# Optimization experiments

Measured on AMD Instinct MI355X. Metric: run time of the kernel, lower is better.

## Reference

```python
import jax, jax.numpy as jnp
import numpy as np

NEG_INF = -jnp.inf


def setup_inputs() -> dict:
    key = jax.random.key(0)
    kq, kk, kv = jax.random.split(key, 3)
    B, L, H, E = 2, 2048, 16, 64
    queries = jax.random.normal(kq, (B, L, H, E), dtype=jnp.float32)
    keys = jax.random.normal(kk, (B, L, H, E), dtype=jnp.float32)
    values = jax.random.normal(kv, (B, L, H, E), dtype=jnp.float32)
    return {"queries": queries, "keys": keys, "values": values}


def reference(queries, keys, values):
    B, L, H, E = queries.shape
    scale = 1.0 / jnp.sqrt(jnp.asarray(E, dtype=queries.dtype))
    # scores: [B, H, L, S]
    scores = jnp.einsum("blhe,bshe->bhls", queries, keys)
    # causal mask: True above the diagonal -> masked out
    causal = jnp.triu(jnp.ones((L, L), dtype=bool), k=1)
    scores = jnp.where(causal[None, None, :, :], NEG_INF, scores)
    A = jax.nn.softmax(scale * scores, axis=-1)
    # output: [B, L, H, D]
    V = jnp.einsum("bhls,bshd->blhd", A, values)
    return V
```

## Files before the change

### kernel.cpp

```cpp
#include <hip/hip_runtime.h>


using f32x4  = __attribute__((ext_vector_type(4))) float;
using bf16x8 = __attribute__((ext_vector_type(8))) short;
using u32x2  = __attribute__((ext_vector_type(2))) unsigned int;
using u32x4  = __attribute__((ext_vector_type(4))) unsigned int;

constexpr int L = 2048;
constexpr int H = 16;
constexpr int E = 64;
constexpr int QBLK = 64;
constexpr int KVBLK = 64;
constexpr float QSC = 0.125f * 1.44269504088896f;
constexpr float THR = 8.0f;

#if defined(__has_builtin)
#if __has_builtin(__builtin_amdgcn_exp2f)
#define HAVE_EXP2 1
#endif
#endif
__device__ __forceinline__ float fexp2(float x) {
#ifdef HAVE_EXP2
    return __builtin_amdgcn_exp2f(x);
#else
    float r;
    asm("v_exp_f32 %0, %1" : "=v"(r) : "v"(x));
    return r;
#endif
}

__device__ __forceinline__ unsigned cvt_pk(float lo, float hi) {
    unsigned r;
    asm("v_cvt_pk_bf16_f32 %0, %1, %2" : "=v"(r) : "v"(lo), "v"(hi));
    return r;
}
__device__ __forceinline__ void pl16(unsigned& a, unsigned& b) {
    asm("v_permlane16_swap_b32 %0, %1" : "+v"(a), "+v"(b));
}
__device__ __forceinline__ void pl32(unsigned& a, unsigned& b) {
    asm("v_permlane32_swap_b32 %0, %1" : "+v"(a), "+v"(b));
}
__device__ __forceinline__ unsigned opaque_copy(unsigned a) {
    unsigned b;
    asm("v_mov_b32 %0, %1" : "=v"(b) : "v"(a));
    return b;
}
__device__ __forceinline__ float gmax4(float x) {
    unsigned a = __float_as_uint(x), b = opaque_copy(a);
    pl16(a, b);
    float m = fmaxf(__uint_as_float(a), __uint_as_float(b));
    unsigned c = __float_as_uint(m), d = opaque_copy(c);
    pl32(c, d);
    return fmaxf(__uint_as_float(c), __uint_as_float(d));
}
__device__ __forceinline__ float gsum4(float x) {
    unsigned a = __float_as_uint(x), b = opaque_copy(a);
    pl16(a, b);
    float s = __uint_as_float(a) + __uint_as_float(b);
    unsigned c = __float_as_uint(s), d = opaque_copy(c);
    pl32(c, d);
    return __uint_as_float(c) + __uint_as_float(d);
}
__device__ __forceinline__ int swz(int row, int bcol) {
    return (row * 128 + bcol) ^ ((row & 7) << 4);
}
__device__ __forceinline__ int swzV(int row, int bcol) {
    return (row * 128 + bcol) ^ ((((row & 7) ^ (row >> 3)) & 7) << 4);
}

__global__ __launch_bounds__(256)
void prep_kernel(const float* __restrict__ K, const float* __restrict__ V,
                 short* __restrict__ Kb, short* __restrict__ Vb)
{
    __shared__ float Vt[64][65];
    const int bx  = blockIdx.x;
    const int t   = bx & 31;
    const int bh  = bx >> 5;
    const int tid = threadIdx.x;
    const size_t bhoff = (size_t)(bh >> 4) * L * (H * E) + (size_t)(bh & 15) * E;
    const size_t tileo = (size_t)(bh * 32 + t) * 4096;

    #pragma unroll
    for (int g = 0; g < 2; ++g) {
        const int c  = g * 256 + tid;
        const int r  = c >> 3;
        const int e0 = (c & 7) * 8;
        const float* kp = K + bhoff + (size_t)(t * 64 + r) * 1024 + e0;
        f32x4 k0 = *(const f32x4*)kp, k1 = *(const f32x4*)(kp + 4);
        u32x4 kt;
        kt[0] = cvt_pk(k0[0], k0[1]); kt[1] = cvt_pk(k0[2], k0[3]);
        kt[2] = cvt_pk(k1[0], k1[1]); kt[3] = cvt_pk(k1[2], k1[3]);
        *(u32x4*)(Kb + tileo + r * 64 + (((e0 >> 3) ^ (r & 7)) * 8)) = kt;
        const float* vp = V + bhoff + (size_t)(t * 64 + r) * 1024 + e0;
        f32x4 v0 = *(const f32x4*)vp, v1 = *(const f32x4*)(vp + 4);
        #pragma unroll
        for (int k2 = 0; k2 < 4; ++k2) { Vt[r][e0 + k2] = v0[k2]; Vt[r][e0 + 4 + k2] = v1[k2]; }
    }
    __syncthreads();
    #pragma unroll
    for (int g = 0; g < 2; ++g) {
        const int c  = g * 256 + tid;
        const int d  = c >> 3;
        const int jp = c & 7;
        const int F  = ((d & 7) ^ (d >> 3)) & 7;
        const int col0 = 8 * (jp ^ F);
        float vals[8];
        #pragma unroll
        for (int i = 0; i < 8; ++i) {
            const int col = col0 + i;
            const int s = 16 * ((col >> 3) & 3) + 8 * (col >> 5) + (col & 7);
            vals[i] = Vt[s][d];
        }
        u32x4 vt;
        vt[0] = cvt_pk(vals[0], vals[1]); vt[1] = cvt_pk(vals[2], vals[3]);
        vt[2] = cvt_pk(vals[4], vals[5]); vt[3] = cvt_pk(vals[6], vals[7]);
        *(u32x4*)(Vb + tileo + d * 64 + jp * 8) = vt;
    }
}

__global__ __launch_bounds__(256, 4)
void fattn_main(const float* __restrict__ Q,
                const short* __restrict__ Kb,
                const short* __restrict__ Vb,
                float* __restrict__ O)
{
    __shared__ short Kl[2][4096];
    __shared__ short Vl[2][4096];

    const int bx  = blockIdx.x;
    const int xcd = bx & 7;
    const int j   = bx >> 3;
    const int bh  = (j & 3) * 8 + xcd;
    const int v_  = j >> 2;
    const int q2  = v_ >> 3, x_ = v_ & 7;
    const int iq  = (q2 & 1) ? (31 - (q2 >> 1) - 2 * x_) : (2 * x_ + (q2 >> 1));
    const int tid = threadIdx.x;
    const int w    = tid >> 6;
    const int lane = tid & 63;
    const int l16  = lane & 15;
    const int lhi  = lane >> 4;

    const size_t bhoff  = (size_t)(bh >> 4) * L * (H * E) + (size_t)(bh & 15) * E;
    const int rs_ = H * E;
    const size_t kvbase = (size_t)bh * 32 * 4096;

    u32x4 kreg[2], vreg[2];
    auto stage_regs = [&](int t) {
        const u32x4* kp = (const u32x4*)(Kb + kvbase + (size_t)t * 4096);
        const u32x4* vp = (const u32x4*)(Vb + kvbase + (size_t)t * 4096);
        #pragma unroll
        for (int g = 0; g < 2; ++g) {
            kreg[g] = kp[g * 256 + tid];
            vreg[g] = vp[g * 256 + tid];
        }
    };
    auto write_stage = [&](int buf) {
        #pragma unroll
        for (int g = 0; g < 2; ++g) {
            ((u32x4*)Kl[buf])[g * 256 + tid] = kreg[g];
            ((u32x4*)Vl[buf])[g * 256 + tid] = vreg[g];
        }
    };

    const int qg = iq * QBLK + w * 16 + l16;
    bf16x8 qf[2];
    {
        const float* qp = Q + bhoff + (size_t)qg * rs_ + lhi * 8;
        #pragma unroll
        for (int kf = 0; kf < 2; ++kf) {
            f32x4 xv = *(const f32x4*)(qp + kf * 32);
            f32x4 yv = *(const f32x4*)(qp + kf * 32 + 4);
            union { u32x4 u; bf16x8 hh; } r;
            r.u[0] = cvt_pk(xv[0] * QSC, xv[1] * QSC);
            r.u[1] = cvt_pk(xv[2] * QSC, xv[3] * QSC);
            r.u[2] = cvt_pk(yv[0] * QSC, yv[1] * QSC);
            r.u[3] = cvt_pk(yv[2] * QSC, yv[3] * QSC);
            qf[kf] = r.hh;
        }
    }

    float m_run = -INFINITY, lsum = 0.0f;
    f32x4 oacc[4];
    #pragma unroll
    for (int dt = 0; dt < 4; ++dt) oacc[dt] = (f32x4){0.f, 0.f, 0.f, 0.f};

    const int total = iq + 1;
    stage_regs(0);
    write_stage(0);
    if (total > 1) stage_regs(1);
    __syncthreads();

    for (int i = 0; i < total; ++i) {
        const char* Kbl = (const char*)Kl[i & 1];
        const char* Vbl = (const char*)Vl[i & 1];

        f32x4 p[4];
        #pragma unroll
        for (int st = 0; st < 4; ++st) p[st] = (f32x4){0.f, 0.f, 0.f, 0.f};
        __builtin_amdgcn_s_setprio(1);
        #pragma unroll
        for (int st = 0; st < 4; ++st) {
            #pragma unroll
            for (int kf = 0; kf < 2; ++kf) {
                bf16x8 af = *(const bf16x8*)(Kbl + swz(st * 16 + l16, (lhi * 8 + kf * 32) * 2));
                p[st] = __builtin_amdgcn_mfma_f32_16x16x32_bf16(af, qf[kf], p[st], 0, 0, 0);
            }
        }
        __builtin_amdgcn_s_setprio(0);

        if (i == total - 1) {
            #pragma unroll
            for (int st = 0; st < 4; ++st)
                #pragma unroll
                for (int r = 0; r < 4; ++r) {
                    const int kg = i * KVBLK + st * 16 + lhi * 4 + r;
                    if (kg > qg) p[st][r] = -INFINITY;
                }
        }

        if (i + 1 < total) write_stage((i + 1) & 1);
        if (i + 2 < total) stage_regs(i + 2);

        f32x4 mv = p[0];
        #pragma unroll
        for (int st = 1; st < 4; ++st)
            #pragma unroll
            for (int r = 0; r < 4; ++r) mv[r] = fmaxf(mv[r], p[st][r]);
        float mx = fmaxf(fmaxf(mv[0], mv[1]), fmaxf(mv[2], mv[3]));
        mx = gmax4(mx);
        if (!__all(mx <= m_run + THR)) {
            const float mn = fmaxf(m_run, mx);
            const float corr = fexp2(m_run - mn);
            lsum *= corr;
            #pragma unroll
            for (int dt = 0; dt < 4; ++dt)
                #pragma unroll
                for (int r = 0; r < 4; ++r) oacc[dt][r] *= corr;
            m_run = mn;
        }
        f32x4 rsv = (f32x4){0.f, 0.f, 0.f, 0.f};
        #pragma unroll
        for (int st = 0; st < 4; ++st)
            #pragma unroll
            for (int r = 0; r < 4; ++r) {
                const float e = fexp2(p[st][r] - m_run);
                p[st][r] = e;
                rsv[r] += e;
            }
        lsum += gsum4((rsv[0] + rsv[1]) + (rsv[2] + rsv[3]));

        unsigned wp[4][2];
        #pragma unroll
        for (int st = 0; st < 4; ++st) {
            wp[st][0] = cvt_pk(p[st][0], p[st][1]);
            wp[st][1] = cvt_pk(p[st][2], p[st][3]);
        }
        #pragma unroll
        for (int hh = 0; hh < 2; ++hh) {
            pl16(wp[0][hh], wp[1][hh]);
            pl16(wp[2][hh], wp[3][hh]);
            pl32(wp[0][hh], wp[2][hh]);
            pl32(wp[1][hh], wp[3][hh]);
        }
        union { u32x4 u; bf16x8 v; } pb0, pb1;
        pb0.u[0] = wp[0][0]; pb0.u[1] = wp[0][1];
        pb0.u[2] = wp[1][0]; pb0.u[3] = wp[1][1];
        pb1.u[0] = wp[2][0]; pb1.u[1] = wp[2][1];
        pb1.u[2] = wp[3][0]; pb1.u[3] = wp[3][1];

        __builtin_amdgcn_s_setprio(1);
        #pragma unroll
        for (int dt = 0; dt < 4; ++dt) {
            bf16x8 vf0 = *(const bf16x8*)(Vbl + swzV(dt * 16 + l16, (lhi * 8) * 2));
            oacc[dt] = __builtin_amdgcn_mfma_f32_16x16x32_bf16(vf0, pb0.v, oacc[dt], 0, 0, 0);
            bf16x8 vf1 = *(const bf16x8*)(Vbl + swzV(dt * 16 + l16, (lhi * 8 + 32) * 2));
            oacc[dt] = __builtin_amdgcn_mfma_f32_16x16x32_bf16(vf1, pb1.v, oacc[dt], 0, 0, 0);
        }
        __builtin_amdgcn_s_setprio(0);

        if (i + 1 < total) __syncthreads();
    }

    const float inv = 1.0f / lsum;
    float* op = O + bhoff + (size_t)qg * rs_;
    #pragma unroll
    for (int dt = 0; dt < 4; ++dt) {
        f32x4 o = oacc[dt];
        o[0] *= inv; o[1] *= inv; o[2] *= inv; o[3] *= inv;
        *(f32x4*)(op + dt * 16 + lhi * 4) = o;
    }
}

__global__ __launch_bounds__(256, 4)
void fattn_fb(const float* __restrict__ Q,
              const float* __restrict__ K,
              const float* __restrict__ V,
              float* __restrict__ O)
{
    __shared__ short Kl[2][KVBLK * 64];
    __shared__ short Vl[2][64 * KVBLK];

    const int bx  = blockIdx.x;
    const int xcd = bx & 7;
    const int j   = bx >> 3;
    const int bh  = (j & 3) * 8 + xcd;
    const int v_  = j >> 2;
    const int q2  = v_ >> 3, x_ = v_ & 7;
    const int iq  = (q2 & 1) ? (31 - (q2 >> 1) - 2 * x_) : (2 * x_ + (q2 >> 1));
    const int tid = threadIdx.x;
    const int w    = tid >> 6;
    const int lane = tid & 63;
    const int l16  = lane & 15;
    const int lhi  = lane >> 4;

    const size_t bhoff = (size_t)(bh >> 4) * L * (H * E) + (size_t)(bh & 15) * E;
    const int rs_ = H * E;
    const int sv0 = (tid >> 4) * 4;
    const int d0  = (tid & 15) * 4;
    const int kc  = ((sv0 >> 3) & 1) * 32 + (sv0 >> 4) * 8 + (sv0 & 7);

    f32x4 ka[2][2];
    f32x4 va[4];
    auto issue_loads = [&](int t) {
        const int sb = t * KVBLK;
        #pragma unroll
        for (int g = 0; g < 2; ++g) {
            const int c = g * 256 + tid;
            const int s = c >> 3;
            const int e0 = (c & 7) * 8;
            const f32x4* kp = (const f32x4*)(K + bhoff + (size_t)(sb + s) * rs_ + e0);
            ka[g][0] = kp[0];
            ka[g][1] = kp[1];
        }
        #pragma unroll
        for (int jj = 0; jj < 4; ++jj)
            va[jj] = *(const f32x4*)(V + bhoff + (size_t)(sb + sv0 + jj) * rs_ + d0);
    };
    auto write_lds = [&](int bufi) {
        short* Kb = Kl[bufi];
        short* Vb = Vl[bufi];
        #pragma unroll
        for (int g = 0; g < 2; ++g) {
            const int c = g * 256 + tid;
            const int s = c >> 3;
            const int e0 = (c & 7) * 8;
            u32x4 kt;
            kt[0] = cvt_pk(ka[g][0][0], ka[g][0][1]);
            kt[1] = cvt_pk(ka[g][0][2], ka[g][0][3]);
            kt[2] = cvt_pk(ka[g][1][0], ka[g][1][1]);
            kt[3] = cvt_pk(ka[g][1][2], ka[g][1][3]);
            *(u32x4*)((char*)Kb + swz(s, e0 * 2)) = kt;
        }
        #pragma unroll
        for (int dd = 0; dd < 4; ++dd) {
            u32x2 vt;
            vt[0] = cvt_pk(va[0][dd], va[1][dd]);
            vt[1] = cvt_pk(va[2][dd], va[3][dd]);
            *(u32x2*)((char*)Vb + swzV(d0 + dd, kc * 2)) = vt;
        }
    };

    const int qg = iq * QBLK + w * 16 + l16;
    bf16x8 qf[2];
    {
        const float* qp = Q + bhoff + (size_t)qg * rs_ + lhi * 8;
        #pragma unroll
        for (int kf = 0; kf < 2; ++kf) {
            f32x4 xv = *(const f32x4*)(qp + kf * 32);
            f32x4 yv = *(const f32x4*)(qp + kf * 32 + 4);
            union { u32x4 u; bf16x8 hh; } r;
            r.u[0] = cvt_pk(xv[0] * QSC, xv[1] * QSC);
            r.u[1] = cvt_pk(xv[2] * QSC, xv[3] * QSC);
            r.u[2] = cvt_pk(yv[0] * QSC, yv[1] * QSC);
            r.u[3] = cvt_pk(yv[2] * QSC, yv[3] * QSC);
            qf[kf] = r.hh;
        }
    }

    float m_run = -INFINITY, lsum = 0.0f;
    f32x4 oacc[4];
    #pragma unroll
    for (int dt = 0; dt < 4; ++dt) oacc[dt] = (f32x4){0.f, 0.f, 0.f, 0.f};

    const int total = iq + 1;
    issue_loads(0);
    write_lds(0);
    if (total > 1) issue_loads(1);
    __syncthreads();

    for (int i = 0; i < total; ++i) {
        const char* Kbl = (const char*)Kl[i & 1];
        const char* Vbl = (const char*)Vl[i & 1];
        f32x4 p[4];
        #pragma unroll
        for (int st = 0; st < 4; ++st) p[st] = (f32x4){0.f, 0.f, 0.f, 0.f};
        __builtin_amdgcn_s_setprio(1);
        #pragma unroll
        for (int st = 0; st < 4; ++st) {
            #pragma unroll
            for (int kf = 0; kf < 2; ++kf) {
                bf16x8 af = *(const bf16x8*)(Kbl + swz(st * 16 + l16, (lhi * 8 + kf * 32) * 2));
                p[st] = __builtin_amdgcn_mfma_f32_16x16x32_bf16(af, qf[kf], p[st], 0, 0, 0);
            }
        }
        __builtin_amdgcn_s_setprio(0);
        if (i == total - 1) {
            #pragma unroll
            for (int st = 0; st < 4; ++st)
                #pragma unroll
                for (int r = 0; r < 4; ++r) {
                    const int kg = i * KVBLK + st * 16 + lhi * 4 + r;
                    if (kg > qg) p[st][r] = -INFINITY;
                }
        }
        if (i + 1 < total) write_lds((i + 1) & 1);
        if (i + 2 < total) issue_loads(i + 2);

        f32x4 mv = p[0];
        #pragma unroll
        for (int st = 1; st < 4; ++st)
            #pragma unroll
            for (int r = 0; r < 4; ++r) mv[r] = fmaxf(mv[r], p[st][r]);
        float mx = fmaxf(fmaxf(mv[0], mv[1]), fmaxf(mv[2], mv[3]));
        mx = gmax4(mx);
        if (!__all(mx <= m_run + THR)) {
            const float mn = fmaxf(m_run, mx);
            const float corr = fexp2(m_run - mn);
            lsum *= corr;
            #pragma unroll
            for (int dt = 0; dt < 4; ++dt)
                #pragma unroll
                for (int r = 0; r < 4; ++r) oacc[dt][r] *= corr;
            m_run = mn;
        }
        f32x4 rsv = (f32x4){0.f, 0.f, 0.f, 0.f};
        #pragma unroll
        for (int st = 0; st < 4; ++st)
            #pragma unroll
            for (int r = 0; r < 4; ++r) {
                const float e = fexp2(p[st][r] - m_run);
                p[st][r] = e;
                rsv[r] += e;
            }
        lsum += gsum4((rsv[0] + rsv[1]) + (rsv[2] + rsv[3]));

        unsigned wp[4][2];
        #pragma unroll
        for (int st = 0; st < 4; ++st) {
            wp[st][0] = cvt_pk(p[st][0], p[st][1]);
            wp[st][1] = cvt_pk(p[st][2], p[st][3]);
        }
        #pragma unroll
        for (int hh = 0; hh < 2; ++hh) {
            pl16(wp[0][hh], wp[1][hh]);
            pl16(wp[2][hh], wp[3][hh]);
            pl32(wp[0][hh], wp[2][hh]);
            pl32(wp[1][hh], wp[3][hh]);
        }
        union { u32x4 u; bf16x8 v; } pb0, pb1;
        pb0.u[0] = wp[0][0]; pb0.u[1] = wp[0][1];
        pb0.u[2] = wp[1][0]; pb0.u[3] = wp[1][1];
        pb1.u[0] = wp[2][0]; pb1.u[1] = wp[2][1];
        pb1.u[2] = wp[3][0]; pb1.u[3] = wp[3][1];

        __builtin_amdgcn_s_setprio(1);
        #pragma unroll
        for (int dt = 0; dt < 4; ++dt) {
            bf16x8 vf0 = *(const bf16x8*)(Vbl + swzV(dt * 16 + l16, (lhi * 8) * 2));
            oacc[dt] = __builtin_amdgcn_mfma_f32_16x16x32_bf16(vf0, pb0.v, oacc[dt], 0, 0, 0);
            bf16x8 vf1 = *(const bf16x8*)(Vbl + swzV(dt * 16 + l16, (lhi * 8 + 32) * 2));
            oacc[dt] = __builtin_amdgcn_mfma_f32_16x16x32_bf16(vf1, pb1.v, oacc[dt], 0, 0, 0);
        }
        __builtin_amdgcn_s_setprio(0);
        if (i + 1 < total) __syncthreads();
    }

    const float inv = 1.0f / lsum;
    float* op = O + bhoff + (size_t)qg * rs_;
    #pragma unroll
    for (int dt = 0; dt < 4; ++dt) {
        f32x4 o = oacc[dt];
        o[0] *= inv; o[1] *= inv; o[2] *= inv; o[3] *= inv;
        *(f32x4*)(op + dt * 16 + lhi * 4) = o;
    }
}

extern "C" void kernel_launch(void* const* d_in, const int* in_sizes, int n_in,
                              void* d_out, int out_size, void* d_ws, size_t ws_size,
                              hipStream_t stream) {
    const float* Q = (const float*)d_in[0];
    const float* K = (const float*)d_in[1];
    const float* V = (const float*)d_in[2];
    float* O = (float*)d_out;
    const size_t kb_elems = (size_t)32 * 32 * 4096;
    if (ws_size >= 2 * kb_elems * sizeof(short)) {
        short* Kb = (short*)d_ws;
        short* Vb = Kb + kb_elems;
        prep_kernel<<<1024, 256, 0, stream>>>(K, V, Kb, Vb);
        fattn_main<<<1024, 256, 0, stream>>>(Q, Kb, Vb, O);
    } else {
        fattn_fb<<<1024, 256, 0, stream>>>(Q, K, V, O);
    }
}
```

Measured before the change: 50.47 us.

## Replace LDS-staged attention kernel with single-wave register-only kernel and paired work units

```diff
diff --git a/kernel.cpp b/kernel.cpp
--- a/kernel.cpp
+++ b/kernel.cpp
@@ -9,7 +9,6 @@
 constexpr int L = 2048;
 constexpr int H = 16;
 constexpr int E = 64;
-constexpr int QBLK = 64;
 constexpr int KVBLK = 64;
 constexpr float QSC = 0.125f * 1.44269504088896f;
 constexpr float THR = 8.0f;
@@ -118,14 +117,181 @@
     }
 }
 
+__global__ __launch_bounds__(64, 2)
+void fattn_nolds(const float* __restrict__ Q,
+                 const short* __restrict__ Kb,
+                 const short* __restrict__ Vb,
+                 float* __restrict__ O)
+{
+    const int bx   = blockIdx.x;
+    const int xcd  = bx & 7;
+    const int j    = bx >> 3;
+    const int bh   = (j >> 6) * 8 + xcd;
+    const int pa   = j & 63;
+    const int lane = threadIdx.x;
+    const int l16  = lane & 15;
+    const int lhi  = lane >> 4;
+
+    const size_t bhoff = (size_t)(bh >> 4) * L * (H * E) + (size_t)(bh & 15) * E;
+    const char* Kt0 = (const char*)(Kb + (size_t)bh * 32 * 4096);
+    const char* Vt0 = (const char*)(Vb + (size_t)bh * 32 * 4096);
+
+    int koff[2];
+    #pragma unroll
+    for (int kf = 0; kf < 2; ++kf)
+        koff[kf] = l16 * 128 + ((lhi * 16 + kf * 64) ^ ((l16 & 7) << 4));
+    int voff[4][2];
+    #pragma unroll
+    for (int dt = 0; dt < 4; ++dt) {
+        const int row = dt * 16 + l16;
+        const int msk = (((row & 7) ^ (row >> 3)) & 7) << 4;
+        #pragma unroll
+        for (int kf = 0; kf < 2; ++kf)
+            voff[dt][kf] = row * 128 + ((lhi * 16 + kf * 64) ^ msk);
+    }
+
+    for (int seg = 0; seg < 2; ++seg) {
+        const int unit = seg ? pa : 127 - pa;
+        const int T    = (unit >> 2) + 1;
+        const int qg   = unit * 16 + l16;
+
+        bf16x8 qf[2];
+        {
+            const float* qp = Q + bhoff + (size_t)qg * (H * E) + lhi * 8;
+            #pragma unroll
+            for (int kf = 0; kf < 2; ++kf) {
+                f32x4 xv = *(const f32x4*)(qp + kf * 32);
+                f32x4 yv = *(const f32x4*)(qp + kf * 32 + 4);
+                union { u32x4 u; bf16x8 hh; } r;
+                r.u[0] = cvt_pk(xv[0] * QSC, xv[1] * QSC);
+                r.u[1] = cvt_pk(xv[2] * QSC, xv[3] * QSC);
+                r.u[2] = cvt_pk(yv[0] * QSC, yv[1] * QSC);
+                r.u[3] = cvt_pk(yv[2] * QSC, yv[3] * QSC);
+                qf[kf] = r.hh;
+            }
+        }
+
+        float m_run = -INFINITY, lsum = 0.0f;
+        f32x4 oacc[4];
+        #pragma unroll
+        for (int dt = 0; dt < 4; ++dt) oacc[dt] = (f32x4){0.f, 0.f, 0.f, 0.f};
+
+        bf16x8 kreg[4][2], vreg[4][2];
+        #pragma unroll
+        for (int st = 0; st < 4; ++st)
+            #pragma unroll
+            for (int kf = 0; kf < 2; ++kf)
+                kreg[st][kf] = *(const bf16x8*)(Kt0 + st * 2048 + koff[kf]);
+
+        for (int t = 0; t < T; ++t) {
+            const char* Vtc = Vt0 + (size_t)t * 8192;
+            #pragma unroll
+            for (int dt = 0; dt < 4; ++dt)
+                #pragma unroll
+                for (int kf = 0; kf < 2; ++kf)
+                    vreg[dt][kf] = *(const bf16x8*)(Vtc + voff[dt][kf]);
+
+            f32x4 p[4];
+            #pragma unroll
+            for (int st = 0; st < 4; ++st) p[st] = (f32x4){0.f, 0.f, 0.f, 0.f};
+            #pragma unroll
+            for (int st = 0; st < 4; ++st)
+                #pragma unroll
+                for (int kf = 0; kf < 2; ++kf)
+                    p[st] = __builtin_amdgcn_mfma_f32_16x16x32_bf16(kreg[st][kf], qf[kf], p[st], 0, 0, 0);
+
+            if (t + 1 < T) {
+                const char* Ktc = Kt0 + (size_t)(t + 1) * 8192;
+                #pragma unroll
+                for (int st = 0; st < 4; ++st)
+                    #pragma unroll
+                    for (int kf = 0; kf < 2; ++kf)
+                        kreg[st][kf] = *(const bf16x8*)(Ktc + st * 2048 + koff[kf]);
+            }
+
+            if (t == T - 1) {
+                #pragma unroll
+                for (int st = 0; st < 4; ++st)
+                    #pragma unroll
+                    for (int r = 0; r < 4; ++r) {
+                        const int kg = t * KVBLK + st * 16 + lhi * 4 + r;
+                        if (kg > qg) p[st][r] = -INFINITY;
+                    }
+            }
+
+            f32x4 mv = p[0];
+            #pragma unroll
+            for (int st = 1; st < 4; ++st)
+                #pragma unroll
+                for (int r = 0; r < 4; ++r) mv[r] = fmaxf(mv[r], p[st][r]);
+            float mx = fmaxf(fmaxf(mv[0], mv[1]), fmaxf(mv[2], mv[3]));
+            mx = gmax4(mx);
+            if (!__all(mx <= m_run + THR)) {
+                const float mn = fmaxf(m_run, mx);
+                const float corr = fexp2(m_run - mn);
+                lsum *= corr;
+                #pragma unroll
+                for (int dt = 0; dt < 4; ++dt)
+                    #pragma unroll
+                    for (int r = 0; r < 4; ++r) oacc[dt][r] *= corr;
+                m_run = mn;
+            }
+            f32x4 rsv = (f32x4){0.f, 0.f, 0.f, 0.f};
+            #pragma unroll
+            for (int st = 0; st < 4; ++st)
+                #pragma unroll
+                for (int r = 0; r < 4; ++r) {
+                    const float e = fexp2(p[st][r] - m_run);
+                    p[st][r] = e;
+                    rsv[r] += e;
+                }
+            lsum += gsum4((rsv[0] + rsv[1]) + (rsv[2] + rsv[3]));
+
+            unsigned wp[4][2];
+            #pragma unroll
+            for (int st = 0; st < 4; ++st) {
+                wp[st][0] = cvt_pk(p[st][0], p[st][1]);
+                wp[st][1] = cvt_pk(p[st][2], p[st][3]);
+            }
+            #pragma unroll
+            for (int hh = 0; hh < 2; ++hh) {
+                pl16(wp[0][hh], wp[1][hh]);
+                pl16(wp[2][hh], wp[3][hh]);
+                pl32(wp[0][hh], wp[2][hh]);
+                pl32(wp[1][hh], wp[3][hh]);
+            }
+            union { u32x4 u; bf16x8 v; } pb0, pb1;
+            pb0.u[0] = wp[0][0]; pb0.u[1] = wp[0][1];
+            pb0.u[2] = wp[1][0]; pb0.u[3] = wp[1][1];
+            pb1.u[0] = wp[2][0]; pb1.u[1] = wp[2][1];
+            pb1.u[2] = wp[3][0]; pb1.u[3] = wp[3][1];
+
+            #pragma unroll
+            for (int dt = 0; dt < 4; ++dt) {
+                oacc[dt] = __builtin_amdgcn_mfma_f32_16x16x32_bf16(vreg[dt][0], pb0.v, oacc[dt], 0, 0, 0);
+                oacc[dt] = __builtin_amdgcn_mfma_f32_16x16x32_bf16(vreg[dt][1], pb1.v, oacc[dt], 0, 0, 0);
+            }
+        }
+
+        const float inv = 1.0f / lsum;
+        float* op = O + bhoff + (size_t)qg * (H * E);
+        #pragma unroll
+        for (int dt = 0; dt < 4; ++dt) {
+            f32x4 o = oacc[dt];
+            o[0] *= inv; o[1] *= inv; o[2] *= inv; o[3] *= inv;
+            *(f32x4*)(op + dt * 16 + lhi * 4) = o;
+        }
+    }
+}
+
 __global__ __launch_bounds__(256, 4)
-void fattn_main(const float* __restrict__ Q,
-                const short* __restrict__ Kb,
-                const short* __restrict__ Vb,
-                float* __restrict__ O)
+void fattn_fb(const float* __restrict__ Q,
+              const float* __restrict__ K,
+              const float* __restrict__ V,
+              float* __restrict__ O)
 {
-    __shared__ short Kl[2][4096];
-    __shared__ short Vl[2][4096];
+    __shared__ short Kl[2][KVBLK * 64];
+    __shared__ short Vl[2][64 * KVBLK];
 
     const int bx  = blockIdx.x;
     const int xcd = bx & 7;
@@ -140,179 +306,6 @@
     const int l16  = lane & 15;
     const int lhi  = lane >> 4;
 
-    const size_t bhoff  = (size_t)(bh >> 4) * L * (H * E) + (size_t)(bh & 15) * E;
-    const int rs_ = H * E;
-    const size_t kvbase = (size_t)bh * 32 * 4096;
-
-    u32x4 kreg[2], vreg[2];
-    auto stage_regs = [&](int t) {
-        const u32x4* kp = (const u32x4*)(Kb + kvbase + (size_t)t * 4096);
-        const u32x4* vp = (const u32x4*)(Vb + kvbase + (size_t)t * 4096);
-        #pragma unroll
-        for (int g = 0; g < 2; ++g) {
-            kreg[g] = kp[g * 256 + tid];
-            vreg[g] = vp[g * 256 + tid];
-        }
-    };
-    auto write_stage = [&](int buf) {
-        #pragma unroll
-        for (int g = 0; g < 2; ++g) {
-            ((u32x4*)Kl[buf])[g * 256 + tid] = kreg[g];
-            ((u32x4*)Vl[buf])[g * 256 + tid] = vreg[g];
-        }
-    };
-
-    const int qg = iq * QBLK + w * 16 + l16;
-    bf16x8 qf[2];
-    {
-        const float* qp = Q + bhoff + (size_t)qg * rs_ + lhi * 8;
-        #pragma unroll
-        for (int kf = 0; kf < 2; ++kf) {
-            f32x4 xv = *(const f32x4*)(qp + kf * 32);
-            f32x4 yv = *(const f32x4*)(qp + kf * 32 + 4);
-            union { u32x4 u; bf16x8 hh; } r;
-            r.u[0] = cvt_pk(xv[0] * QSC, xv[1] * QSC);
-            r.u[1] = cvt_pk(xv[2] * QSC, xv[3] * QSC);
-            r.u[2] = cvt_pk(yv[0] * QSC, yv[1] * QSC);
-            r.u[3] = cvt_pk(yv[2] * QSC, yv[3] * QSC);
-            qf[kf] = r.hh;
-        }
-    }
-
-    float m_run = -INFINITY, lsum = 0.0f;
-    f32x4 oacc[4];
-    #pragma unroll
-    for (int dt = 0; dt < 4; ++dt) oacc[dt] = (f32x4){0.f, 0.f, 0.f, 0.f};
-
-    const int total = iq + 1;
-    stage_regs(0);
-    write_stage(0);
-    if (total > 1) stage_regs(1);
-    __syncthreads();
-
-    for (int i = 0; i < total; ++i) {
-        const char* Kbl = (const char*)Kl[i & 1];
-        const char* Vbl = (const char*)Vl[i & 1];
-
-        f32x4 p[4];
-        #pragma unroll
-        for (int st = 0; st < 4; ++st) p[st] = (f32x4){0.f, 0.f, 0.f, 0.f};
-        __builtin_amdgcn_s_setprio(1);
-        #pragma unroll
-        for (int st = 0; st < 4; ++st) {
-            #pragma unroll
-            for (int kf = 0; kf < 2; ++kf) {
-                bf16x8 af = *(const bf16x8*)(Kbl + swz(st * 16 + l16, (lhi * 8 + kf * 32) * 2));
-                p[st] = __builtin_amdgcn_mfma_f32_16x16x32_bf16(af, qf[kf], p[st], 0, 0, 0);
-            }
-        }
-        __builtin_amdgcn_s_setprio(0);
-
-        if (i == total - 1) {
-            #pragma unroll
-            for (int st = 0; st < 4; ++st)
-                #pragma unroll
-                for (int r = 0; r < 4; ++r) {
-                    const int kg = i * KVBLK + st * 16 + lhi * 4 + r;
-                    if (kg > qg) p[st][r] = -INFINITY;
-                }
-        }
-
-        if (i + 1 < total) write_stage((i + 1) & 1);
-        if (i + 2 < total) stage_regs(i + 2);
-
-        f32x4 mv = p[0];
-        #pragma unroll
-        for (int st = 1; st < 4; ++st)
-            #pragma unroll
-            for (int r = 0; r < 4; ++r) mv[r] = fmaxf(mv[r], p[st][r]);
-        float mx = fmaxf(fmaxf(mv[0], mv[1]), fmaxf(mv[2], mv[3]));
-        mx = gmax4(mx);
-        if (!__all(mx <= m_run + THR)) {
-            const float mn = fmaxf(m_run, mx);
-            const float corr = fexp2(m_run - mn);
-            lsum *= corr;
-            #pragma unroll
-            for (int dt = 0; dt < 4; ++dt)
-                #pragma unroll
-                for (int r = 0; r < 4; ++r) oacc[dt][r] *= corr;
-            m_run = mn;
-        }
-        f32x4 rsv = (f32x4){0.f, 0.f, 0.f, 0.f};
-        #pragma unroll
-        for (int st = 0; st < 4; ++st)
-            #pragma unroll
-            for (int r = 0; r < 4; ++r) {
-                const float e = fexp2(p[st][r] - m_run);
-                p[st][r] = e;
-                rsv[r] += e;
-            }
-        lsum += gsum4((rsv[0] + rsv[1]) + (rsv[2] + rsv[3]));
-
-        unsigned wp[4][2];
-        #pragma unroll
-        for (int st = 0; st < 4; ++st) {
-            wp[st][0] = cvt_pk(p[st][0], p[st][1]);
-            wp[st][1] = cvt_pk(p[st][2], p[st][3]);
-        }
-        #pragma unroll
-        for (int hh = 0; hh < 2; ++hh) {
-            pl16(wp[0][hh], wp[1][hh]);
-            pl16(wp[2][hh], wp[3][hh]);
-            pl32(wp[0][hh], wp[2][hh]);
-            pl32(wp[1][hh], wp[3][hh]);
-        }
-        union { u32x4 u; bf16x8 v; } pb0, pb1;
-        pb0.u[0] = wp[0][0]; pb0.u[1] = wp[0][1];
-        pb0.u[2] = wp[1][0]; pb0.u[3] = wp[1][1];
-        pb1.u[0] = wp[2][0]; pb1.u[1] = wp[2][1];
-        pb1.u[2] = wp[3][0]; pb1.u[3] = wp[3][1];
-
-        __builtin_amdgcn_s_setprio(1);
-        #pragma unroll
-        for (int dt = 0; dt < 4; ++dt) {
-            bf16x8 vf0 = *(const bf16x8*)(Vbl + swzV(dt * 16 + l16, (lhi * 8) * 2));
-            oacc[dt] = __builtin_amdgcn_mfma_f32_16x16x32_bf16(vf0, pb0.v, oacc[dt], 0, 0, 0);
-            bf16x8 vf1 = *(const bf16x8*)(Vbl + swzV(dt * 16 + l16, (lhi * 8 + 32) * 2));
-            oacc[dt] = __builtin_amdgcn_mfma_f32_16x16x32_bf16(vf1, pb1.v, oacc[dt], 0, 0, 0);
-        }
-        __builtin_amdgcn_s_setprio(0);
-
-        if (i + 1 < total) __syncthreads();
-    }
-
-    const float inv = 1.0f / lsum;
-    float* op = O + bhoff + (size_t)qg * rs_;
-    #pragma unroll
-    for (int dt = 0; dt < 4; ++dt) {
-        f32x4 o = oacc[dt];
-        o[0] *= inv; o[1] *= inv; o[2] *= inv; o[3] *= inv;
-        *(f32x4*)(op + dt * 16 + lhi * 4) = o;
-    }
-}
-
-__global__ __launch_bounds__(256, 4)
-void fattn_fb(const float* __restrict__ Q,
-              const float* __restrict__ K,
-              const float* __restrict__ V,
-              float* __restrict__ O)
-{
-    __shared__ short Kl[2][KVBLK * 64];
-    __shared__ short Vl[2][64 * KVBLK];
-
-    const int bx  = blockIdx.x;
-    const int xcd = bx & 7;
-    const int j   = bx >> 3;
-    const int bh  = (j & 3) * 8 + xcd;
-    const int v_  = j >> 2;
-    const int q2  = v_ >> 3, x_ = v_ & 7;
-    const int iq  = (q2 & 1) ? (31 - (q2 >> 1) - 2 * x_) : (2 * x_ + (q2 >> 1));
-    const int tid = threadIdx.x;
-    const int w    = tid >> 6;
-    const int lane = tid & 63;
-    const int l16  = lane & 15;
-    const int lhi  = lane >> 4;
-
     const size_t bhoff = (size_t)(bh >> 4) * L * (H * E) + (size_t)(bh & 15) * E;
     const int rs_ = H * E;
     const int sv0 = (tid >> 4) * 4;
@@ -360,7 +353,7 @@
         }
     };
 
-    const int qg = iq * QBLK + w * 16 + l16;
+    const int qg = iq * 64 + w * 16 + l16;
     bf16x8 qf[2];
     {
         const float* qp = Q + bhoff + (size_t)qg * rs_ + lhi * 8;
@@ -394,7 +387,6 @@
         f32x4 p[4];
         #pragma unroll
         for (int st = 0; st < 4; ++st) p[st] = (f32x4){0.f, 0.f, 0.f, 0.f};
-        __builtin_amdgcn_s_setprio(1);
         #pragma unroll
         for (int st = 0; st < 4; ++st) {
             #pragma unroll
@@ -403,7 +395,6 @@
                 p[st] = __builtin_amdgcn_mfma_f32_16x16x32_bf16(af, qf[kf], p[st], 0, 0, 0);
             }
         }
-        __builtin_amdgcn_s_setprio(0);
         if (i == total - 1) {
             #pragma unroll
             for (int st = 0; st < 4; ++st)
@@ -463,7 +454,6 @@
         pb1.u[0] = wp[2][0]; pb1.u[1] = wp[2][1];
         pb1.u[2] = wp[3][0]; pb1.u[3] = wp[3][1];
 
-        __builtin_amdgcn_s_setprio(1);
         #pragma unroll
         for (int dt = 0; dt < 4; ++dt) {
             bf16x8 vf0 = *(const bf16x8*)(Vbl + swzV(dt * 16 + l16, (lhi * 8) * 2));
@@ -471,7 +461,6 @@
             bf16x8 vf1 = *(const bf16x8*)(Vbl + swzV(dt * 16 + l16, (lhi * 8 + 32) * 2));
             oacc[dt] = __builtin_amdgcn_mfma_f32_16x16x32_bf16(vf1, pb1.v, oacc[dt], 0, 0, 0);
         }
-        __builtin_amdgcn_s_setprio(0);
         if (i + 1 < total) __syncthreads();
     }
 
@@ -497,7 +486,7 @@
         short* Kb = (short*)d_ws;
         short* Vb = Kb + kb_elems;
         prep_kernel<<<1024, 256, 0, stream>>>(K, V, Kb, Vb);
-        fattn_main<<<1024, 256, 0, stream>>>(Q, Kb, Vb, O);
+        fattn_nolds<<<2048, 64, 0, stream>>>(Q, Kb, Vb, O);
     } else {
         fattn_fb<<<1024, 256, 0, stream>>>(Q, K, V, O);
     }
```

Result: slower. 66.56 us (+31.9%).

## Stage K/V tiles via direct global-to-LDS loads instead of register staging

Applied to the files above, without the earlier changes.

```diff
diff --git a/kernel.cpp b/kernel.cpp
--- a/kernel.cpp
+++ b/kernel.cpp
@@ -9,7 +9,6 @@
 constexpr int L = 2048;
 constexpr int H = 16;
 constexpr int E = 64;
-constexpr int QBLK = 64;
 constexpr int KVBLK = 64;
 constexpr float QSC = 0.125f * 1.44269504088896f;
 constexpr float THR = 8.0f;
@@ -67,6 +66,11 @@
 __device__ __forceinline__ int swzV(int row, int bcol) {
     return (row * 128 + bcol) ^ ((((row & 7) ^ (row >> 3)) & 7) << 4);
 }
+__device__ __forceinline__ void gload16(const short* g, short* l) {
+    __builtin_amdgcn_global_load_lds(
+        (const __attribute__((address_space(1))) void*)g,
+        (__attribute__((address_space(3))) void*)l, 16, 0, 0);
+}
 
 __global__ __launch_bounds__(256)
 void prep_kernel(const float* __restrict__ K, const float* __restrict__ V,
@@ -144,25 +148,20 @@
     const int rs_ = H * E;
     const size_t kvbase = (size_t)bh * 32 * 4096;
 
-    u32x4 kreg[2], vreg[2];
-    auto stage_regs = [&](int t) {
-        const u32x4* kp = (const u32x4*)(Kb + kvbase + (size_t)t * 4096);
-        const u32x4* vp = (const u32x4*)(Vb + kvbase + (size_t)t * 4096);
-        #pragma unroll
-        for (int g = 0; g < 2; ++g) {
-            kreg[g] = kp[g * 256 + tid];
-            vreg[g] = vp[g * 256 + tid];
-        }
+    const int wboff = w * 2048 + lane * 16;
+    const int wlds  = w * 2048;
+
+    auto stage = [&](int t, int buf) {
+        const char* kt = (const char*)(Kb + kvbase) + (size_t)t * 8192 + wboff;
+        const char* vt = (const char*)(Vb + kvbase) + (size_t)t * 8192 + wboff;
+        gload16((const short*)kt,          Kl[buf] + wlds / 2);
+        gload16((const short*)(kt + 1024), Kl[buf] + (wlds + 1024) / 2);
+        gload16((const short*)vt,          Vl[buf] + wlds / 2);
+        gload16((const short*)(vt + 1024), Vl[buf] + (wlds + 1024) / 2);
     };
-    auto write_stage = [&](int buf) {
-        #pragma unroll
-        for (int g = 0; g < 2; ++g) {
-            ((u32x4*)Kl[buf])[g * 256 + tid] = kreg[g];
-            ((u32x4*)Vl[buf])[g * 256 + tid] = vreg[g];
-        }
-    };
-
-    const int qg = iq * QBLK + w * 16 + l16;
+
+    const int qg = iq * 64 + w * 16 + l16;
+    stage(0, 0);
     bf16x8 qf[2];
     {
         const float* qp = Q + bhoff + (size_t)qg * rs_ + lhi * 8;
@@ -185,12 +184,14 @@
     for (int dt = 0; dt < 4; ++dt) oacc[dt] = (f32x4){0.f, 0.f, 0.f, 0.f};
 
     const int total = iq + 1;
-    stage_regs(0);
-    write_stage(0);
-    if (total > 1) stage_regs(1);
-    __syncthreads();
+    __builtin_amdgcn_sched_barrier(0);
+    asm volatile("s_waitcnt vmcnt(0)" ::: "memory");
+    __builtin_amdgcn_s_barrier();
+    __builtin_amdgcn_sched_barrier(0);
 
     for (int i = 0; i < total; ++i) {
+        if (i + 1 < total) stage(i + 1, (i + 1) & 1);
+
         const char* Kbl = (const char*)Kl[i & 1];
         const char* Vbl = (const char*)Vl[i & 1];
 
@@ -217,9 +218,6 @@
                     if (kg > qg) p[st][r] = -INFINITY;
                 }
         }
-
-        if (i + 1 < total) write_stage((i + 1) & 1);
-        if (i + 2 < total) stage_regs(i + 2);
 
         f32x4 mv = p[0];
         #pragma unroll
@@ -278,7 +276,12 @@
         }
         __builtin_amdgcn_s_setprio(0);
 
-        if (i + 1 < total) __syncthreads();
+        if (i + 1 < total) {
+            __builtin_amdgcn_sched_barrier(0);
+            asm volatile("s_waitcnt vmcnt(0)" ::: "memory");
+            __builtin_amdgcn_s_barrier();
+            __builtin_amdgcn_sched_barrier(0);
+        }
     }
 
     const float inv = 1.0f / lsum;
@@ -360,7 +363,7 @@
         }
     };
 
-    const int qg = iq * QBLK + w * 16 + l16;
+    const int qg = iq * 64 + w * 16 + l16;
     bf16x8 qf[2];
     {
         const float* qp = Q + bhoff + (size_t)qg * rs_ + lhi * 8;
@@ -394,7 +397,6 @@
         f32x4 p[4];
         #pragma unroll
         for (int st = 0; st < 4; ++st) p[st] = (f32x4){0.f, 0.f, 0.f, 0.f};
-        __builtin_amdgcn_s_setprio(1);
         #pragma unroll
         for (int st = 0; st < 4; ++st) {
             #pragma unroll
@@ -403,7 +405,6 @@
                 p[st] = __builtin_amdgcn_mfma_f32_16x16x32_bf16(af, qf[kf], p[st], 0, 0, 0);
             }
         }
-        __builtin_amdgcn_s_setprio(0);
         if (i == total - 1) {
             #pragma unroll
             for (int st = 0; st < 4; ++st)
@@ -463,7 +464,6 @@
         pb1.u[0] = wp[2][0]; pb1.u[1] = wp[2][1];
         pb1.u[2] = wp[3][0]; pb1.u[3] = wp[3][1];
 
-        __builtin_amdgcn_s_setprio(1);
         #pragma unroll
         for (int dt = 0; dt < 4; ++dt) {
             bf16x8 vf0 = *(const bf16x8*)(Vbl + swzV(dt * 16 + l16, (lhi * 8) * 2));
@@ -471,7 +471,6 @@
             bf16x8 vf1 = *(const bf16x8*)(Vbl + swzV(dt * 16 + l16, (lhi * 8 + 32) * 2));
             oacc[dt] = __builtin_amdgcn_mfma_f32_16x16x32_bf16(vf1, pb1.v, oacc[dt], 0, 0, 0);
         }
-        __builtin_amdgcn_s_setprio(0);
         if (i + 1 < total) __syncthreads();
     }
 
```

New measurement: 52.53 us. 4.1% more time.
